# Performance work log

Hardware: AMD Instinct MI355X
Metric: run time of the kernel (lower is better)

Reference implementation:

```python
import jax, jax.numpy as jnp
import numpy as np

PATCH = 3
ALPHA = 0.1

def unfold_patches(f, p):
    # Emulates F.unfold with zero padding p//2, stride 1: [B,C,H,W] -> [B, C*p*p, H, W].
    # Descriptor-dim ordering differs from torch's, but the correlation sum over the
    # descriptor dim is permutation-invariant, so the output is identical.
    pad = p // 2
    B, C, H, W = f.shape
    fp = jnp.pad(f, ((0, 0), (0, 0), (pad, pad), (pad, pad)))
    patches = [fp[:, :, i:i + H, j:j + W] for i in range(p) for j in range(p)]
    return jnp.concatenate(patches, axis=1)


def setup_inputs() -> dict:
    key = jax.random.key(0)
    k1, k2 = jax.random.split(key)
    x_rgb = jax.random.uniform(k1, (4, 3, 64, 64), dtype=jnp.float32)
    feature = jax.random.normal(k2, (4, 64, 64, 64), dtype=jnp.float32)
    return {"x_rgb": x_rgb, "feature": feature}


def reference(x_rgb, feature):
    B, _, H, W = x_rgb.shape
    HW = H * W
    rgb = x_rgb.reshape(B, 3, HW).transpose(0, 2, 1)            # [B, HW, 3]
    local = unfold_patches(feature, PATCH).reshape(B, -1, HW)    # [B, D, HW], D = C*p*p
    # correlation = K^T K over descriptor dim -> [B, HW, HW]
    corr = jnp.einsum('bdp,bdq->bpq', local, local)
    attn = jax.nn.softmax(corr / ALPHA, axis=-1)
    weighted = jnp.einsum('bpq,bqc->bpc', attn, rgb)             # [B, HW, 3]
    return weighted.transpose(0, 2, 1).reshape(B, 3, H, W)
```

## Files before the change

kernel.cpp:

```cpp
#include <hip/hip_runtime.h>
#include <hip/hip_bf16.h>

typedef __attribute__((ext_vector_type(4))) float f32x4;
typedef __attribute__((ext_vector_type(8))) int i32x8;

constexpr int kB = 4, kC = 64, kH = 64, kW = 64;
constexpr int kHW = kH * kW;
constexpr int kD  = kC * 9;
constexpr int KSPLIT = 8;
constexpr int KBLK = 16;
constexpr int QWAVE = 32;
constexpr int QWG = 128;
constexpr int NTILE = kHW / KSPLIT / KBLK;
constexpr int ROWB8 = 640;
constexpr int TILEB = KBLK * ROWB8;
constexpr int TCHUNK = TILEB / 16;

#define FSCALE 3.79828370f
#define FS2    14.4269504089f
#define SEED_SLACK 64.0f
#define SCL1 0x7F7F7F7F

__global__ __launch_bounds__(256)
void nlwa_selfsq(const float* __restrict__ feat, float* __restrict__ sq) {
    int idx = blockIdx.x * 256 + threadIdx.x;
    if (idx >= kB * kHW) return;
    int b = idx >> 12, p = idx & 4095;
    const float* f = feat + (size_t)b * kC * kHW + p;
    float s = 0.f;
    #pragma unroll 8
    for (int c = 0; c < kC; ++c) { float v = f[c * kHW]; s = fmaf(v, v, s); }
    sq[idx] = s;
}

__global__ __launch_bounds__(256)
void nlwa_unfold(const float* __restrict__ feat, unsigned char* __restrict__ Kd) {
    int idx = blockIdx.x * 256 + threadIdx.x;
    if (idx >= kB * kHW * (ROWB8 / 8)) return;
    int piece = idx % (ROWB8 / 8);
    int v = (idx / (ROWB8 / 8)) % kHW;
    int b = idx / ((ROWB8 / 8) * kHW);
    unsigned long long pack = 0ULL;
    if (piece < 72) {
        int y0 = v >> 6, x0 = v & 63;
        #pragma unroll
        for (int j = 0; j < 8; ++j) {
            int d = piece * 8 + j;
            int c = d / 9, dl = d % 9;
            int y = y0 + dl / 3 - 1;
            int x = x0 + dl % 3 - 1;
            float val = 0.f;
            if ((unsigned)y < 64u && (unsigned)x < 64u)
                val = feat[((b * kC + c) * kH + y) * kW + x] * FSCALE;
            unsigned int fb = __builtin_bit_cast(unsigned int, val * 0x1p-120f);
            unsigned int mag = ((fb & 0x7fffffffu) + 0x80000u) >> 20;
            if (mag > 0x7eu) mag = 0x7eu;
            unsigned long long u8 = ((fb >> 31) << 7) | mag;
            pack |= u8 << (8 * j);
        }
    }
    int c16 = piece >> 1, half = piece & 1;
    int cp = c16 ^ (v & 7);
    *(unsigned long long*)(Kd + (size_t)(b * kHW + v) * ROWB8 + cp * 16 + half * 8) = pack;
}

__global__ __launch_bounds__(256, 4)
void nlwa_attn(const unsigned char* __restrict__ Kd,
               const float* __restrict__ rgb,
               const float* __restrict__ sq,
               float* __restrict__ part) {
    __shared__ alignas(16) unsigned char Ks[2][KBLK][ROWB8];

    int orig = blockIdx.x;
    int wg = (orig & 7) * 128 + (orig >> 3);
    int qblk = wg & 31;
    int pr = wg >> 5;
    int ks = pr & 7;
    int b  = pr >> 3;

    int tid = threadIdx.x, lane = tid & 63, wid = tid >> 6;
    int lr = lane & 15, lg = lane >> 4;
    int s7 = lr & 7;
    int qwave = qblk * QWG + wid * QWAVE;
    int k0 = ks * (kHW / KSPLIT);

    i32x8 qb[2][5];
    #pragma unroll
    for (int g = 0; g < 2; ++g) {
        int qrow = qwave + g * 16 + lr;
        const unsigned char* qbase = Kd + (size_t)(b * kHW + qrow) * ROWB8;
        int sq7 = qrow & 7;
        #pragma unroll
        for (int W = 0; W < 5; ++W) {
            int4 lo = *(const int4*)(qbase + W * 128 + (((lg * 2)     ^ sq7) << 4));
            int4 hi = *(const int4*)(qbase + W * 128 + (((lg * 2 + 1) ^ sq7) << 4));
            qb[g][W] = (i32x8){lo.x, lo.y, lo.z, lo.w, hi.x, hi.y, hi.z, hi.w};
        }
    }

    float m[2], l[2] = {0.f, 0.f};
    float O[2][3] = {{0,0,0},{0,0,0}};
    const float* sqb = sq + b * kHW;
    #pragma unroll
    for (int g = 0; g < 2; ++g) {
        int q = qwave + g * 16 + lr, y = q >> 6, x = q & 63;
        float s = 0.f;
        #pragma unroll
        for (int dy = -1; dy <= 1; ++dy)
            #pragma unroll
            for (int dx = -1; dx <= 1; ++dx) {
                int yy = y + dy, xx = x + dx;
                if ((unsigned)yy < 64u && (unsigned)xx < 64u) s += sqb[yy * 64 + xx];
            }
        m[g] = s * FS2 - SEED_SLACK;
    }

    const unsigned char* ksrc = Kd + (size_t)(b * kHW + k0) * ROWB8;
    unsigned char* lds0 = &Ks[0][0][0];

    auto stage = [&](int t, int bufi) {
        const unsigned char* src = ksrc + (size_t)t * TILEB;
        unsigned char* dstb = lds0 + bufi * TILEB;
        #pragma unroll
        for (int it = 0; it < 3; ++it) {
            int base = it * 256 + wid * 64;
            if (base < TCHUNK) {
                __builtin_amdgcn_global_load_lds(
                    (const __attribute__((address_space(1))) void*)(src + (size_t)(base + lane) * 16),
                    (__attribute__((address_space(3))) void*)(dstb + (size_t)base * 16),
                    16, 0, 0);
            }
        }
    };

    stage(0, 0);
    __syncthreads();

    int eA = lr * ROWB8 + (((lg * 2)     ^ s7) << 4);
    int eB = lr * ROWB8 + (((lg * 2 + 1) ^ s7) << 4);

    int buf = 0;
    for (int t = 0; t < NTILE; ++t) {
        if (t + 1 < NTILE) stage(t + 1, buf ^ 1);

        const unsigned char* kb = lds0 + buf * TILEB;
        f32x4 acc[2];
        acc[0] = (f32x4){0.f, 0.f, 0.f, 0.f};
        acc[1] = (f32x4){0.f, 0.f, 0.f, 0.f};

        #pragma unroll
        for (int W = 0; W < 5; ++W) {
            int4 lo = *(const int4*)(kb + eA + W * 128);
            int4 hi = *(const int4*)(kb + eB + W * 128);
            i32x8 a = (i32x8){lo.x, lo.y, lo.z, lo.w, hi.x, hi.y, hi.z, hi.w};
            acc[0] = __builtin_amdgcn_mfma_scale_f32_16x16x128_f8f6f4(
                        a, qb[0][W], acc[0], 0, 0, 0, SCL1, 0, SCL1);
            acc[1] = __builtin_amdgcn_mfma_scale_f32_16x16x128_f8f6f4(
                        a, qb[1][W], acc[1], 0, 0, 0, SCL1, 0, SCL1);
        }

        float pm[2];
        #pragma unroll
        for (int g = 0; g < 2; ++g)
            pm[g] = fmaxf(fmaxf(acc[g][0], acc[g][1]), fmaxf(acc[g][2], acc[g][3]));

        float dmx = fmaxf(pm[0] - m[0], pm[1] - m[1]);
        if (__any(dmx >= -25.f)) {
            int kt0 = k0 + t * KBLK;
            #pragma unroll
            for (int g = 0; g < 2; ++g) {
                float v = pm[g];
                v = fmaxf(v, __shfl_xor(v, 16));
                v = fmaxf(v, __shfl_xor(v, 32));
                float mn = fmaxf(m[g], v);
                float al = exp2f(m[g] - mn);
                m[g] = mn;
                l[g] *= al;
                O[g][0] *= al; O[g][1] *= al; O[g][2] *= al;
            }
            float4 rv[3];
            #pragma unroll
            for (int c = 0; c < 3; ++c)
                rv[c] = *(const float4*)(rgb + (size_t)(b * 3 + c) * kHW + kt0 + lg * 4);
            #pragma unroll
            for (int g = 0; g < 2; ++g) {
                float p0 = exp2f(acc[g][0] - m[g]);
                float p1 = exp2f(acc[g][1] - m[g]);
                float p2 = exp2f(acc[g][2] - m[g]);
                float p3 = exp2f(acc[g][3] - m[g]);
                l[g] += p0 + p1 + p2 + p3;
                #pragma unroll
                for (int c = 0; c < 3; ++c)
                    O[g][c] += p0 * rv[c].x + p1 * rv[c].y + p2 * rv[c].z + p3 * rv[c].w;
            }
        }
        __syncthreads();
        buf ^= 1;
    }

    #pragma unroll
    for (int g = 0; g < 2; ++g) {
        l[g] += __shfl_xor(l[g], 16); l[g] += __shfl_xor(l[g], 32);
        #pragma unroll
        for (int c = 0; c < 3; ++c) {
            O[g][c] += __shfl_xor(O[g][c], 16);
            O[g][c] += __shfl_xor(O[g][c], 32);
        }
    }
    if (lg == 0) {
        #pragma unroll
        for (int g = 0; g < 2; ++g) {
            int q = qwave + g * 16 + lr;
            float* p = part + ((size_t)(b * kHW + q) * KSPLIT + ks) * 5;
            p[0] = m[g]; p[1] = l[g]; p[2] = O[g][0]; p[3] = O[g][1]; p[4] = O[g][2];
        }
    }
}

__global__ __launch_bounds__(256)
void nlwa_merge(const float* __restrict__ part, float* __restrict__ out) {
    int idx = blockIdx.x * 256 + threadIdx.x;
    if (idx >= kB * kHW) return;
    int b = idx >> 12, q = idx & 4095;
    const float* p = part + (size_t)idx * KSPLIT * 5;
    float M = -INFINITY;
    #pragma unroll
    for (int s = 0; s < KSPLIT; ++s) M = fmaxf(M, p[s * 5]);
    float L = 0.f, o0 = 0.f, o1 = 0.f, o2 = 0.f;
    #pragma unroll
    for (int s = 0; s < KSPLIT; ++s) {
        float a = exp2f(p[s * 5] - M);
        L  += p[s * 5 + 1] * a;
        o0 += p[s * 5 + 2] * a;
        o1 += p[s * 5 + 3] * a;
        o2 += p[s * 5 + 4] * a;
    }
    float inv = 1.f / L;
    out[(b * 3 + 0) * kHW + q] = o0 * inv;
    out[(b * 3 + 1) * kHW + q] = o1 * inv;
    out[(b * 3 + 2) * kHW + q] = o2 * inv;
}

__global__ __launch_bounds__(64)
void nlwa_naive(const float* __restrict__ feat, const float* __restrict__ rgb,
                float* __restrict__ out) {
    int p = blockIdx.x, b = blockIdx.y;
    int pi = p >> 6, pj = p & 63;
    int t = threadIdx.x;
    __shared__ float pdesc[kD];
    __shared__ float rows[kC][3][kW];
    __shared__ float red[64][5];

    for (int d = t; d < kD; d += 64) {
        int c = d / 9, dl = d % 9;
        int y = pi + dl / 3 - 1, x = pj + dl % 3 - 1;
        pdesc[d] = ((unsigned)y < 64u && (unsigned)x < 64u)
                 ? feat[((b * kC + c) * kH + y) * kW + x] : 0.f;
    }
    float m = -INFINITY, l = 0.f, O0 = 0.f, O1 = 0.f, O2 = 0.f;
    for (int qi = 0; qi < kH; ++qi) {
        __syncthreads();
        for (int f = t; f < kC * 3 * kW; f += 64) {
            int x = f & 63, yy = (f >> 6) % 3, c = f / (3 * kW);
            int y = qi + yy - 1;
            rows[c][yy][x] = ((unsigned)y < 64u) ? feat[((b * kC + c) * kH + y) * kW + x] : 0.f;
        }
        __syncthreads();
        float s = 0.f;
        for (int c = 0; c < kC; ++c)
            for (int dl = 0; dl < 9; ++dl) {
                int x = t + dl % 3 - 1;
                float fv = ((unsigned)x < 64u) ? rows[c][dl / 3][x] : 0.f;
                s += pdesc[c * 9 + dl] * fv;
            }
        s *= 14.4269504089f;
        int q = qi * 64 + t;
        float mn = fmaxf(m, s);
        float al = exp2f(m - mn);
        float pv = exp2f(s - mn);
        l = l * al + pv;
        O0 = O0 * al + pv * rgb[(b * 3 + 0) * kHW + q];
        O1 = O1 * al + pv * rgb[(b * 3 + 1) * kHW + q];
        O2 = O2 * al + pv * rgb[(b * 3 + 2) * kHW + q];
        m = mn;
    }
    red[t][0] = m; red[t][1] = l; red[t][2] = O0; red[t][3] = O1; red[t][4] = O2;
    __syncthreads();
    if (t == 0) {
        float M = -INFINITY;
        for (int i = 0; i < 64; ++i) M = fmaxf(M, red[i][0]);
        float L = 0, A = 0, Bv = 0, Cv = 0;
        for (int i = 0; i < 64; ++i) {
            float a = exp2f(red[i][0] - M);
            L += red[i][1] * a; A += red[i][2] * a; Bv += red[i][3] * a; Cv += red[i][4] * a;
        }
        out[(b * 3 + 0) * kHW + p] = A / L;
        out[(b * 3 + 1) * kHW + p] = Bv / L;
        out[(b * 3 + 2) * kHW + p] = Cv / L;
    }
}

extern "C" void kernel_launch(void* const* d_in, const int* in_sizes, int n_in,
                              void* d_out, int out_size, void* d_ws, size_t ws_size,
                              hipStream_t stream) {
    const float* x_rgb   = (const float*)d_in[0];
    const float* feature = (const float*)d_in[1];
    float* out = (float*)d_out;

    size_t needK = (size_t)kB * kHW * ROWB8;
    size_t needP = (size_t)kB * kHW * KSPLIT * 5 * 4;
    size_t needS = (size_t)kB * kHW * 4;
    if (ws_size >= needK + needP + needS) {
        unsigned char* Kd = (unsigned char*)d_ws;
        float* partb = (float*)((char*)d_ws + needK);
        float* sqb   = (float*)((char*)d_ws + needK + needP);
        int pieces = kB * kHW * (ROWB8 / 8);
        nlwa_selfsq<<<(kB * kHW + 255) / 256, 256, 0, stream>>>(feature, sqb);
        nlwa_unfold<<<(pieces + 255) / 256, 256, 0, stream>>>(feature, Kd);
        nlwa_attn<<<kB * (kHW / QWG) * KSPLIT, 256, 0, stream>>>(Kd, x_rgb, sqb, partb);
        nlwa_merge<<<(kB * kHW + 255) / 256, 256, 0, stream>>>(partb, out);
    } else {
        nlwa_naive<<<dim3(kHW, kB), 64, 0, stream>>>(feature, x_rgb, out);
    }
}
```

Measured before the change: 97.66 us.

## Widen attention waves to 64 queries, compute softmax seed from FP8 diagonal

Each wave now processes 64 query rows (four MFMA groups) against every staged key tile, doubling reuse of the LDS key fragments, and workgroups cover 256 queries. Rows are padded to 768 bytes with a 32-byte swizzle so each key/query fragment is loaded as one 32-byte vector. The separate self-norm kernel is removed; the initial running max is derived from the quantized FP8 query self-dot with a smaller slack. In exchange the kernel uses more registers (occupancy hint lowered to 2 blocks/CU), launches half as many workgroups, and the tighter seed may trigger more rescale passes.

```diff
diff --git a/kernel.cpp b/kernel.cpp
--- a/kernel.cpp
+++ b/kernel.cpp
@@ -9,37 +9,24 @@
 constexpr int kD  = kC * 9;
 constexpr int KSPLIT = 8;
 constexpr int KBLK = 16;
-constexpr int QWAVE = 32;
-constexpr int QWG = 128;
+constexpr int QWAVE = 64;
+constexpr int QWG = 256;
 constexpr int NTILE = kHW / KSPLIT / KBLK;
-constexpr int ROWB8 = 640;
-constexpr int TILEB = KBLK * ROWB8;
+constexpr int ROWB = 768;
+constexpr int TILEB = KBLK * ROWB;
 constexpr int TCHUNK = TILEB / 16;
 
 #define FSCALE 3.79828370f
-#define FS2    14.4269504089f
-#define SEED_SLACK 64.0f
+#define SEED_SLACK 8.0f
 #define SCL1 0x7F7F7F7F
-
-__global__ __launch_bounds__(256)
-void nlwa_selfsq(const float* __restrict__ feat, float* __restrict__ sq) {
-    int idx = blockIdx.x * 256 + threadIdx.x;
-    if (idx >= kB * kHW) return;
-    int b = idx >> 12, p = idx & 4095;
-    const float* f = feat + (size_t)b * kC * kHW + p;
-    float s = 0.f;
-    #pragma unroll 8
-    for (int c = 0; c < kC; ++c) { float v = f[c * kHW]; s = fmaf(v, v, s); }
-    sq[idx] = s;
-}
 
 __global__ __launch_bounds__(256)
 void nlwa_unfold(const float* __restrict__ feat, unsigned char* __restrict__ Kd) {
     int idx = blockIdx.x * 256 + threadIdx.x;
-    if (idx >= kB * kHW * (ROWB8 / 8)) return;
-    int piece = idx % (ROWB8 / 8);
-    int v = (idx / (ROWB8 / 8)) % kHW;
-    int b = idx / ((ROWB8 / 8) * kHW);
+    if (idx >= kB * kHW * (ROWB / 8)) return;
+    int piece = idx % (ROWB / 8);
+    int v = (idx / (ROWB / 8)) % kHW;
+    int b = idx / ((ROWB / 8) * kHW);
     unsigned long long pack = 0ULL;
     if (piece < 72) {
         int y0 = v >> 6, x0 = v & 63;
@@ -59,63 +46,64 @@
             pack |= u8 << (8 * j);
         }
     }
-    int c16 = piece >> 1, half = piece & 1;
-    int cp = c16 ^ (v & 7);
-    *(unsigned long long*)(Kd + (size_t)(b * kHW + v) * ROWB8 + cp * 16 + half * 8) = pack;
-}
-
-__global__ __launch_bounds__(256, 4)
+    int c32 = piece >> 2, slot = piece & 3;
+    int cp = c32 ^ (v & 7);
+    *(unsigned long long*)(Kd + (size_t)(b * kHW + v) * ROWB + cp * 32 + slot * 8) = pack;
+}
+
+__global__ __launch_bounds__(256, 2)
 void nlwa_attn(const unsigned char* __restrict__ Kd,
                const float* __restrict__ rgb,
-               const float* __restrict__ sq,
                float* __restrict__ part) {
-    __shared__ alignas(16) unsigned char Ks[2][KBLK][ROWB8];
+    __shared__ alignas(16) unsigned char Ks[2][KBLK][ROWB];
 
     int orig = blockIdx.x;
-    int wg = (orig & 7) * 128 + (orig >> 3);
-    int qblk = wg & 31;
-    int pr = wg >> 5;
+    int wg = (orig & 7) * 64 + (orig >> 3);
+    int qblk = wg & 15;
+    int pr = wg >> 4;
     int ks = pr & 7;
     int b  = pr >> 3;
 
     int tid = threadIdx.x, lane = tid & 63, wid = tid >> 6;
     int lr = lane & 15, lg = lane >> 4;
     int s7 = lr & 7;
+    int lo2 = s7 & 3, h = s7 >> 2;
     int qwave = qblk * QWG + wid * QWAVE;
     int k0 = ks * (kHW / KSPLIT);
 
-    i32x8 qb[2][5];
-    #pragma unroll
-    for (int g = 0; g < 2; ++g) {
-        int qrow = qwave + g * 16 + lr;
-        const unsigned char* qbase = Kd + (size_t)(b * kHW + qrow) * ROWB8;
-        int sq7 = qrow & 7;
-        #pragma unroll
-        for (int W = 0; W < 5; ++W) {
-            int4 lo = *(const int4*)(qbase + W * 128 + (((lg * 2)     ^ sq7) << 4));
-            int4 hi = *(const int4*)(qbase + W * 128 + (((lg * 2 + 1) ^ sq7) << 4));
-            qb[g][W] = (i32x8){lo.x, lo.y, lo.z, lo.w, hi.x, hi.y, hi.z, hi.w};
-        }
-    }
-
-    float m[2], l[2] = {0.f, 0.f};
-    float O[2][3] = {{0,0,0},{0,0,0}};
-    const float* sqb = sq + b * kHW;
-    #pragma unroll
-    for (int g = 0; g < 2; ++g) {
-        int q = qwave + g * 16 + lr, y = q >> 6, x = q & 63;
-        float s = 0.f;
-        #pragma unroll
-        for (int dy = -1; dy <= 1; ++dy)
+    i32x8 qb[4][5];
+    #pragma unroll
+    for (int g = 0; g < 4; ++g) {
+        const unsigned char* qbase = Kd + (size_t)(b * kHW + qwave + g * 16 + lr) * ROWB
+                                   + ((lg ^ lo2) << 5);
+        #pragma unroll
+        for (int W = 0; W < 5; ++W)
+            qb[g][W] = *(const i32x8*)(qbase + ((W ^ h) << 7));
+    }
+
+    float m[4], l[4] = {0.f, 0.f, 0.f, 0.f};
+    float O[4][3] = {{0,0,0},{0,0,0},{0,0,0},{0,0,0}};
+    #pragma unroll
+    for (int g = 0; g < 4; ++g) {
+        float ss = 0.f;
+        #pragma unroll
+        for (int W = 0; W < 5; ++W)
             #pragma unroll
-            for (int dx = -1; dx <= 1; ++dx) {
-                int yy = y + dy, xx = x + dx;
-                if ((unsigned)yy < 64u && (unsigned)xx < 64u) s += sqb[yy * 64 + xx];
+            for (int j = 0; j < 8; ++j) {
+                unsigned int w32 = (unsigned int)qb[g][W][j];
+                #pragma unroll
+                for (int byi = 0; byi < 4; ++byi) {
+                    unsigned int mag = (w32 >> (8 * byi)) & 0x7fu;
+                    float v = __builtin_bit_cast(float, mag << 20) * 0x1p120f;
+                    ss = fmaf(v, v, ss);
+                }
             }
-        m[g] = s * FS2 - SEED_SLACK;
-    }
-
-    const unsigned char* ksrc = Kd + (size_t)(b * kHW + k0) * ROWB8;
+        ss += __shfl_xor(ss, 16);
+        ss += __shfl_xor(ss, 32);
+        m[g] = ss - SEED_SLACK;
+    }
+
+    const unsigned char* ksrc = Kd + (size_t)(b * kHW + k0) * ROWB;
     unsigned char* lds0 = &Ks[0][0][0];
 
     auto stage = [&](int t, int bufi) {
@@ -124,51 +112,53 @@
         #pragma unroll
         for (int it = 0; it < 3; ++it) {
             int base = it * 256 + wid * 64;
-            if (base < TCHUNK) {
-                __builtin_amdgcn_global_load_lds(
-                    (const __attribute__((address_space(1))) void*)(src + (size_t)(base + lane) * 16),
-                    (__attribute__((address_space(3))) void*)(dstb + (size_t)base * 16),
-                    16, 0, 0);
-            }
+            __builtin_amdgcn_global_load_lds(
+                (const __attribute__((address_space(1))) void*)(src + (size_t)(base + lane) * 16),
+                (__attribute__((address_space(3))) void*)(dstb + (size_t)base * 16),
+                16, 0, 0);
         }
     };
 
     stage(0, 0);
     __syncthreads();
 
-    int eA = lr * ROWB8 + (((lg * 2)     ^ s7) << 4);
-    int eB = lr * ROWB8 + (((lg * 2 + 1) ^ s7) << 4);
+    int eBase = lr * ROWB + ((lg ^ lo2) << 5);
+    int eE = eBase + h * 128;
+    int eO = eBase - h * 128;
 
     int buf = 0;
     for (int t = 0; t < NTILE; ++t) {
         if (t + 1 < NTILE) stage(t + 1, buf ^ 1);
 
         const unsigned char* kb = lds0 + buf * TILEB;
-        f32x4 acc[2];
-        acc[0] = (f32x4){0.f, 0.f, 0.f, 0.f};
-        acc[1] = (f32x4){0.f, 0.f, 0.f, 0.f};
+        f32x4 acc[4];
+        #pragma unroll
+        for (int g = 0; g < 4; ++g) acc[g] = (f32x4){0.f, 0.f, 0.f, 0.f};
 
         #pragma unroll
         for (int W = 0; W < 5; ++W) {
-            int4 lo = *(const int4*)(kb + eA + W * 128);
-            int4 hi = *(const int4*)(kb + eB + W * 128);
-            i32x8 a = (i32x8){lo.x, lo.y, lo.z, lo.w, hi.x, hi.y, hi.z, hi.w};
+            i32x8 a = *(const i32x8*)(kb + ((W & 1) ? eO : eE) + W * 128);
             acc[0] = __builtin_amdgcn_mfma_scale_f32_16x16x128_f8f6f4(
                         a, qb[0][W], acc[0], 0, 0, 0, SCL1, 0, SCL1);
             acc[1] = __builtin_amdgcn_mfma_scale_f32_16x16x128_f8f6f4(
                         a, qb[1][W], acc[1], 0, 0, 0, SCL1, 0, SCL1);
-        }
-
-        float pm[2];
-        #pragma unroll
-        for (int g = 0; g < 2; ++g)
+            acc[2] = __builtin_amdgcn_mfma_scale_f32_16x16x128_f8f6f4(
+                        a, qb[2][W], acc[2], 0, 0, 0, SCL1, 0, SCL1);
+            acc[3] = __builtin_amdgcn_mfma_scale_f32_16x16x128_f8f6f4(
+                        a, qb[3][W], acc[3], 0, 0, 0, SCL1, 0, SCL1);
+        }
+
+        float pm[4];
+        #pragma unroll
+        for (int g = 0; g < 4; ++g)
             pm[g] = fmaxf(fmaxf(acc[g][0], acc[g][1]), fmaxf(acc[g][2], acc[g][3]));
 
-        float dmx = fmaxf(pm[0] - m[0], pm[1] - m[1]);
+        float dmx = fmaxf(fmaxf(pm[0] - m[0], pm[1] - m[1]),
+                          fmaxf(pm[2] - m[2], pm[3] - m[3]));
         if (__any(dmx >= -25.f)) {
             int kt0 = k0 + t * KBLK;
             #pragma unroll
-            for (int g = 0; g < 2; ++g) {
+            for (int g = 0; g < 4; ++g) {
                 float v = pm[g];
                 v = fmaxf(v, __shfl_xor(v, 16));
                 v = fmaxf(v, __shfl_xor(v, 32));
@@ -183,7 +173,7 @@
             for (int c = 0; c < 3; ++c)
                 rv[c] = *(const float4*)(rgb + (size_t)(b * 3 + c) * kHW + kt0 + lg * 4);
             #pragma unroll
-            for (int g = 0; g < 2; ++g) {
+            for (int g = 0; g < 4; ++g) {
                 float p0 = exp2f(acc[g][0] - m[g]);
                 float p1 = exp2f(acc[g][1] - m[g]);
                 float p2 = exp2f(acc[g][2] - m[g]);
@@ -199,7 +189,7 @@
     }
 
     #pragma unroll
-    for (int g = 0; g < 2; ++g) {
+    for (int g = 0; g < 4; ++g) {
         l[g] += __shfl_xor(l[g], 16); l[g] += __shfl_xor(l[g], 32);
         #pragma unroll
         for (int c = 0; c < 3; ++c) {
@@ -209,7 +199,7 @@
     }
     if (lg == 0) {
         #pragma unroll
-        for (int g = 0; g < 2; ++g) {
+        for (int g = 0; g < 4; ++g) {
             int q = qwave + g * 16 + lr;
             float* p = part + ((size_t)(b * kHW + q) * KSPLIT + ks) * 5;
             p[0] = m[g]; p[1] = l[g]; p[2] = O[g][0]; p[3] = O[g][1]; p[4] = O[g][2];
@@ -307,17 +297,14 @@
     const float* feature = (const float*)d_in[1];
     float* out = (float*)d_out;
 
-    size_t needK = (size_t)kB * kHW * ROWB8;
+    size_t needK = (size_t)kB * kHW * ROWB;
     size_t needP = (size_t)kB * kHW * KSPLIT * 5 * 4;
-    size_t needS = (size_t)kB * kHW * 4;
-    if (ws_size >= needK + needP + needS) {
+    if (ws_size >= needK + needP) {
         unsigned char* Kd = (unsigned char*)d_ws;
         float* partb = (float*)((char*)d_ws + needK);
-        float* sqb   = (float*)((char*)d_ws + needK + needP);
-        int pieces = kB * kHW * (ROWB8 / 8);
-        nlwa_selfsq<<<(kB * kHW + 255) / 256, 256, 0, stream>>>(feature, sqb);
+        int pieces = kB * kHW * (ROWB / 8);
         nlwa_unfold<<<(pieces + 255) / 256, 256, 0, stream>>>(feature, Kd);
-        nlwa_attn<<<kB * (kHW / QWG) * KSPLIT, 256, 0, stream>>>(Kd, x_rgb, sqb, partb);
+        nlwa_attn<<<kB * (kHW / QWG) * KSPLIT, 256, 0, stream>>>(Kd, x_rgb, partb);
         nlwa_merge<<<(kB * kHW + 255) / 256, 256, 0, stream>>>(partb, out);
     } else {
         nlwa_naive<<<dim3(kHW, kB), 64, 0, stream>>>(feature, x_rgb, out);
```

New measurement: 94.91 us. -2.8%, faster.

## Switch to fp8 16x16x32 MFMA, larger tiles, and compute seed max in-kernel

Applied to the files above, without the earlier changes.

Replaces the scaled 16x16x128 f8f6f4 MFMA with plain fp8 16x16x32 MFMAs over 9 slices of the 576-dim descriptor, skipping the zero padding to 640 bytes. The unfold layout and XOR swizzle change to match. The key tile doubles to 32 rows and workgroups grow to 512 threads (8 waves, 256 queries), so each staged LDS tile is reused by more queries. The separate self-square kernel is removed; the running-max seed is now computed from the quantized query bytes inside the attention kernel, with a smaller slack. The risks are higher register pressure and more MFMA issue slots per tile.

```diff
diff --git a/kernel.cpp b/kernel.cpp
--- a/kernel.cpp
+++ b/kernel.cpp
@@ -2,36 +2,22 @@
 #include <hip/hip_bf16.h>
 
 typedef __attribute__((ext_vector_type(4))) float f32x4;
-typedef __attribute__((ext_vector_type(8))) int i32x8;
+typedef __attribute__((ext_vector_type(2))) long long l64x2;
 
 constexpr int kB = 4, kC = 64, kH = 64, kW = 64;
 constexpr int kHW = kH * kW;
 constexpr int kD  = kC * 9;
 constexpr int KSPLIT = 8;
-constexpr int KBLK = 16;
+constexpr int KBLK = 32;
 constexpr int QWAVE = 32;
-constexpr int QWG = 128;
+constexpr int QWG = 256;
 constexpr int NTILE = kHW / KSPLIT / KBLK;
 constexpr int ROWB8 = 640;
 constexpr int TILEB = KBLK * ROWB8;
 constexpr int TCHUNK = TILEB / 16;
 
 #define FSCALE 3.79828370f
-#define FS2    14.4269504089f
-#define SEED_SLACK 64.0f
-#define SCL1 0x7F7F7F7F
-
-__global__ __launch_bounds__(256)
-void nlwa_selfsq(const float* __restrict__ feat, float* __restrict__ sq) {
-    int idx = blockIdx.x * 256 + threadIdx.x;
-    if (idx >= kB * kHW) return;
-    int b = idx >> 12, p = idx & 4095;
-    const float* f = feat + (size_t)b * kC * kHW + p;
-    float s = 0.f;
-    #pragma unroll 8
-    for (int c = 0; c < kC; ++c) { float v = f[c * kHW]; s = fmaf(v, v, s); }
-    sq[idx] = s;
-}
+#define SEED_SLACK 8.0f
 
 __global__ __launch_bounds__(256)
 void nlwa_unfold(const float* __restrict__ feat, unsigned char* __restrict__ Kd) {
@@ -59,22 +45,22 @@
             pack |= u8 << (8 * j);
         }
     }
-    int c16 = piece >> 1, half = piece & 1;
-    int cp = c16 ^ (v & 7);
+    int c = (piece >> 3) * 4 + (piece & 3);
+    int half = (piece >> 2) & 1;
+    int cp = c ^ (v & 7);
     *(unsigned long long*)(Kd + (size_t)(b * kHW + v) * ROWB8 + cp * 16 + half * 8) = pack;
 }
 
-__global__ __launch_bounds__(256, 4)
+__global__ __launch_bounds__(512, 2)
 void nlwa_attn(const unsigned char* __restrict__ Kd,
                const float* __restrict__ rgb,
-               const float* __restrict__ sq,
                float* __restrict__ part) {
     __shared__ alignas(16) unsigned char Ks[2][KBLK][ROWB8];
 
     int orig = blockIdx.x;
-    int wg = (orig & 7) * 128 + (orig >> 3);
-    int qblk = wg & 31;
-    int pr = wg >> 5;
+    int wg = (orig & 7) * 64 + (orig >> 3);
+    int qblk = wg & 15;
+    int pr = wg >> 4;
     int ks = pr & 7;
     int b  = pr >> 3;
 
@@ -84,35 +70,37 @@
     int qwave = qblk * QWG + wid * QWAVE;
     int k0 = ks * (kHW / KSPLIT);
 
-    i32x8 qb[2][5];
+    int4 qb[2][9];
     #pragma unroll
     for (int g = 0; g < 2; ++g) {
-        int qrow = qwave + g * 16 + lr;
-        const unsigned char* qbase = Kd + (size_t)(b * kHW + qrow) * ROWB8;
-        int sq7 = qrow & 7;
-        #pragma unroll
-        for (int W = 0; W < 5; ++W) {
-            int4 lo = *(const int4*)(qbase + W * 128 + (((lg * 2)     ^ sq7) << 4));
-            int4 hi = *(const int4*)(qbase + W * 128 + (((lg * 2 + 1) ^ sq7) << 4));
-            qb[g][W] = (i32x8){lo.x, lo.y, lo.z, lo.w, hi.x, hi.y, hi.z, hi.w};
-        }
+        const unsigned char* qbase = Kd + (size_t)(b * kHW + qwave + g * 16 + lr) * ROWB8;
+        #pragma unroll
+        for (int p = 0; p < 9; ++p)
+            qb[g][p] = *(const int4*)(qbase + (((p * 4 + lg) ^ s7) << 4));
     }
 
     float m[2], l[2] = {0.f, 0.f};
     float O[2][3] = {{0,0,0},{0,0,0}};
-    const float* sqb = sq + b * kHW;
     #pragma unroll
     for (int g = 0; g < 2; ++g) {
-        int q = qwave + g * 16 + lr, y = q >> 6, x = q & 63;
-        float s = 0.f;
-        #pragma unroll
-        for (int dy = -1; dy <= 1; ++dy)
-            #pragma unroll
-            for (int dx = -1; dx <= 1; ++dx) {
-                int yy = y + dy, xx = x + dx;
-                if ((unsigned)yy < 64u && (unsigned)xx < 64u) s += sqb[yy * 64 + xx];
-            }
-        m[g] = s * FS2 - SEED_SLACK;
+        float ss = 0.f;
+        #pragma unroll
+        for (int p = 0; p < 9; ++p) {
+            const int* w4 = (const int*)&qb[g][p];
+            #pragma unroll
+            for (int j = 0; j < 4; ++j) {
+                unsigned int w32 = (unsigned int)w4[j];
+                #pragma unroll
+                for (int byi = 0; byi < 4; ++byi) {
+                    unsigned int mag = (w32 >> (8 * byi)) & 0x7fu;
+                    float v = __builtin_bit_cast(float, mag << 20) * 0x1p120f;
+                    ss = fmaf(v, v, ss);
+                }
+            }
+        }
+        ss += __shfl_xor(ss, 16);
+        ss += __shfl_xor(ss, 32);
+        m[g] = ss - SEED_SLACK;
     }
 
     const unsigned char* ksrc = Kd + (size_t)(b * kHW + k0) * ROWB8;
@@ -123,7 +111,7 @@
         unsigned char* dstb = lds0 + bufi * TILEB;
         #pragma unroll
         for (int it = 0; it < 3; ++it) {
-            int base = it * 256 + wid * 64;
+            int base = it * 512 + wid * 64;
             if (base < TCHUNK) {
                 __builtin_amdgcn_global_load_lds(
                     (const __attribute__((address_space(1))) void*)(src + (size_t)(base + lane) * 16),
@@ -136,33 +124,47 @@
     stage(0, 0);
     __syncthreads();
 
-    int eA = lr * ROWB8 + (((lg * 2)     ^ s7) << 4);
-    int eB = lr * ROWB8 + (((lg * 2 + 1) ^ s7) << 4);
+    int lo2 = s7 & 3, h = s7 >> 2;
+    int r0 = lr * ROWB8 + ((lg ^ lo2) << 4);
+    int e0 = r0 + h * 64, o0 = r0 - h * 64;
 
     int buf = 0;
     for (int t = 0; t < NTILE; ++t) {
         if (t + 1 < NTILE) stage(t + 1, buf ^ 1);
 
         const unsigned char* kb = lds0 + buf * TILEB;
-        f32x4 acc[2];
-        acc[0] = (f32x4){0.f, 0.f, 0.f, 0.f};
-        acc[1] = (f32x4){0.f, 0.f, 0.f, 0.f};
-
-        #pragma unroll
-        for (int W = 0; W < 5; ++W) {
-            int4 lo = *(const int4*)(kb + eA + W * 128);
-            int4 hi = *(const int4*)(kb + eB + W * 128);
-            i32x8 a = (i32x8){lo.x, lo.y, lo.z, lo.w, hi.x, hi.y, hi.z, hi.w};
-            acc[0] = __builtin_amdgcn_mfma_scale_f32_16x16x128_f8f6f4(
-                        a, qb[0][W], acc[0], 0, 0, 0, SCL1, 0, SCL1);
-            acc[1] = __builtin_amdgcn_mfma_scale_f32_16x16x128_f8f6f4(
-                        a, qb[1][W], acc[1], 0, 0, 0, SCL1, 0, SCL1);
+        f32x4 acc[2][2];
+        #pragma unroll
+        for (int g = 0; g < 2; ++g) {
+            acc[g][0] = (f32x4){0.f, 0.f, 0.f, 0.f};
+            acc[g][1] = (f32x4){0.f, 0.f, 0.f, 0.f};
+        }
+
+        #pragma unroll
+        for (int p = 0; p < 9; ++p) {
+            int off = ((p & 1) ? o0 : e0) + p * 64;
+            int4 ka = *(const int4*)(kb + off);
+            int4 kc = *(const int4*)(kb + 16 * ROWB8 + off);
+            l64x2 ka64 = __builtin_bit_cast(l64x2, ka);
+            l64x2 kc64 = __builtin_bit_cast(l64x2, kc);
+            #pragma unroll
+            for (int w01 = 0; w01 < 2; ++w01) {
+                long long a0 = ka64[w01], a1 = kc64[w01];
+                #pragma unroll
+                for (int g = 0; g < 2; ++g) {
+                    long long bq = __builtin_bit_cast(l64x2, qb[g][p])[w01];
+                    acc[g][0] = __builtin_amdgcn_mfma_f32_16x16x32_fp8_fp8(a0, bq, acc[g][0], 0, 0, 0);
+                    acc[g][1] = __builtin_amdgcn_mfma_f32_16x16x32_fp8_fp8(a1, bq, acc[g][1], 0, 0, 0);
+                }
+            }
         }
 
         float pm[2];
         #pragma unroll
         for (int g = 0; g < 2; ++g)
-            pm[g] = fmaxf(fmaxf(acc[g][0], acc[g][1]), fmaxf(acc[g][2], acc[g][3]));
+            pm[g] = fmaxf(
+                fmaxf(fmaxf(acc[g][0][0], acc[g][0][1]), fmaxf(acc[g][0][2], acc[g][0][3])),
+                fmaxf(fmaxf(acc[g][1][0], acc[g][1][1]), fmaxf(acc[g][1][2], acc[g][1][3])));
 
         float dmx = fmaxf(pm[0] - m[0], pm[1] - m[1]);
         if (__any(dmx >= -25.f)) {
@@ -178,20 +180,26 @@
                 l[g] *= al;
                 O[g][0] *= al; O[g][1] *= al; O[g][2] *= al;
             }
-            float4 rv[3];
-            #pragma unroll
-            for (int c = 0; c < 3; ++c)
-                rv[c] = *(const float4*)(rgb + (size_t)(b * 3 + c) * kHW + kt0 + lg * 4);
-            #pragma unroll
-            for (int g = 0; g < 2; ++g) {
-                float p0 = exp2f(acc[g][0] - m[g]);
-                float p1 = exp2f(acc[g][1] - m[g]);
-                float p2 = exp2f(acc[g][2] - m[g]);
-                float p3 = exp2f(acc[g][3] - m[g]);
-                l[g] += p0 + p1 + p2 + p3;
+            float4 rv[2][3];
+            #pragma unroll
+            for (int s = 0; s < 2; ++s)
                 #pragma unroll
                 for (int c = 0; c < 3; ++c)
-                    O[g][c] += p0 * rv[c].x + p1 * rv[c].y + p2 * rv[c].z + p3 * rv[c].w;
+                    rv[s][c] = *(const float4*)(rgb + (size_t)(b * 3 + c) * kHW + kt0 + s * 16 + lg * 4);
+            #pragma unroll
+            for (int g = 0; g < 2; ++g) {
+                #pragma unroll
+                for (int s = 0; s < 2; ++s) {
+                    float p0 = exp2f(acc[g][s][0] - m[g]);
+                    float p1 = exp2f(acc[g][s][1] - m[g]);
+                    float p2 = exp2f(acc[g][s][2] - m[g]);
+                    float p3 = exp2f(acc[g][s][3] - m[g]);
+                    l[g] += p0 + p1 + p2 + p3;
+                    #pragma unroll
+                    for (int c = 0; c < 3; ++c)
+                        O[g][c] += p0 * rv[s][c].x + p1 * rv[s][c].y
+                                 + p2 * rv[s][c].z + p3 * rv[s][c].w;
+                }
             }
         }
         __syncthreads();
@@ -309,15 +317,12 @@
 
     size_t needK = (size_t)kB * kHW * ROWB8;
     size_t needP = (size_t)kB * kHW * KSPLIT * 5 * 4;
-    size_t needS = (size_t)kB * kHW * 4;
-    if (ws_size >= needK + needP + needS) {
+    if (ws_size >= needK + needP) {
         unsigned char* Kd = (unsigned char*)d_ws;
         float* partb = (float*)((char*)d_ws + needK);
-        float* sqb   = (float*)((char*)d_ws + needK + needP);
         int pieces = kB * kHW * (ROWB8 / 8);
-        nlwa_selfsq<<<(kB * kHW + 255) / 256, 256, 0, stream>>>(feature, sqb);
         nlwa_unfold<<<(pieces + 255) / 256, 256, 0, stream>>>(feature, Kd);
-        nlwa_attn<<<kB * (kHW / QWG) * KSPLIT, 256, 0, stream>>>(Kd, x_rgb, sqb, partb);
+        nlwa_attn<<<kB * (kHW / QWG) * KSPLIT, 512, 0, stream>>>(Kd, x_rgb, partb);
         nlwa_merge<<<(kB * kHW + 255) / 256, 256, 0, stream>>>(partb, out);
     } else {
         nlwa_naive<<<dim3(kHW, kB), 64, 0, stream>>>(feature, x_rgb, out);
```

Result: faster. 92.83 us (-4.9%).
